# Kernel tuning notes

Hardware: AMD Instinct MI355X
Metric: run time of the kernel (lower is better)

## Reference

```python
import jax, jax.numpy as jnp
import numpy as np

NUM_ITER = 5
DIM = 512
BATCH = 64


def setup_inputs() -> dict:
    key = jax.random.key(0)
    a = jax.random.normal(key, (BATCH, DIM, DIM), dtype=jnp.float32)
    # Symmetric PSD input (covariance-like), as in bilinear pooling; Newton-Schulz
    # requires SPD matrices for convergence.
    x = jnp.einsum('bik,bjk->bij', a, a) / DIM
    I = jnp.eye(DIM, dtype=jnp.float32)
    return {"x": x, "I": I}


def reference(x, I):
    # x: [bs, dim, dim]; I: [dim, dim]
    normA = jnp.sqrt(jnp.sum(x * x, axis=(1, 2), keepdims=True))  # Frobenius norm per matrix
    Y = x / normA
    bs, dim, _ = x.shape
    Z = jnp.broadcast_to(I, (bs, dim, dim))
    Ib = Z
    for _ in range(NUM_ITER):
        T = 0.5 * (3.0 * Ib - jnp.matmul(Z, Y))
        Y = jnp.matmul(Y, T)
        Z = jnp.matmul(T, Z)
    sA = Y * jnp.sqrt(normA)
    return sA
```

## Files before the change

kernel.cpp:

```cpp
#include <hip/hip_runtime.h>
#include <hip/hip_bf16.h>
#include <stdint.h>

#define DIM   512
#define BATCH 64
#define KENC  1024
#define BM    128
#define BN    128
#define BKT   32
#define NKT   16

typedef __attribute__((ext_vector_type(8))) short short8;
typedef __attribute__((ext_vector_type(4))) float floatx4;

__device__ __forceinline__ ushort f2bf(float f) {
    __hip_bfloat16 h = __float2bfloat16(f);
    return *(ushort*)&h;
}
__device__ __forceinline__ float bf2f(ushort u) {
    __hip_bfloat16 h = *(__hip_bfloat16*)&u;
    return (float)h;
}

typedef __attribute__((address_space(3))) uint32_t lds_u32;
typedef const __attribute__((address_space(1))) uint32_t glb_u32;
__device__ __forceinline__ void gload16(const ushort* g, ushort* l) {
    __builtin_amdgcn_global_load_lds((glb_u32*)g, (lds_u32*)l, 16, 0, 0);
}

__global__ __launch_bounds__(256) void norm_partial_kernel(const float* __restrict__ x,
                                                           float* __restrict__ partial) {
    int b = blockIdx.y;
    int i = blockIdx.x;
    const float4* xv = (const float4*)(x + (size_t)b * DIM * DIM + (size_t)i * (DIM * DIM / 16));
    float s = 0.f;
    #pragma unroll
    for (int r = 0; r < 16; ++r) {
        float4 v = xv[r * 256 + threadIdx.x];
        s += v.x * v.x + v.y * v.y + v.z * v.z + v.w * v.w;
    }
    #pragma unroll
    for (int off = 32; off > 0; off >>= 1) s += __shfl_down(s, off, 64);
    __shared__ float red[4];
    int lane = threadIdx.x & 63, wid = threadIdx.x >> 6;
    if (lane == 0) red[wid] = s;
    __syncthreads();
    if (threadIdx.x == 0) partial[b * 16 + i] = red[0] + red[1] + red[2] + red[3];
}

__global__ __launch_bounds__(256) void init_kernel(const float* __restrict__ x,
                                                   const float* __restrict__ partial,
                                                   float* __restrict__ norms,
                                                   ushort* __restrict__ Yenc,
                                                   ushort* __restrict__ Tenc) {
    int b = blockIdx.y;
    float s = 0.f;
    #pragma unroll
    for (int p = 0; p < 16; ++p) s += partial[b * 16 + p];
    float nrm = sqrtf(s);
    if (blockIdx.x == 0 && threadIdx.x == 0) norms[b] = nrm;
    float inv = 1.0f / nrm;
    int idx = (blockIdx.x * 256 + threadIdx.x) * 4;
    int r = idx >> 9;
    int c = idx & 511;
    float4 v = *(const float4*)(x + (size_t)b * DIM * DIM + idx);
    float yv[4] = {v.x * inv, v.y * inv, v.z * inv, v.w * inv};
    size_t base = (size_t)b * DIM * KENC + (size_t)r * KENC;
    ushort yhi[4], ylo[4], thi[4], tlo[4];
    #pragma unroll
    for (int j = 0; j < 4; ++j) {
        float y = yv[j];
        yhi[j] = f2bf(y);
        ylo[j] = f2bf(y - bf2f(yhi[j]));
        float t = ((c + j) == r ? 1.5f : 0.0f) - 0.5f * y;
        thi[j] = f2bf(t);
        tlo[j] = f2bf(t - bf2f(thi[j]));
    }
    *(ushort4*)(Yenc + base + c)       = *(ushort4*)yhi;
    *(ushort4*)(Yenc + base + 512 + c) = *(ushort4*)ylo;
    *(ushort4*)(Tenc + base + c)       = *(ushort4*)thi;
    *(ushort4*)(Tenc + base + 512 + c) = *(ushort4*)tlo;
}

__device__ __forceinline__ void gemm_core(const ushort* Ag, const ushort* Bg,
                                          ushort* sm, floatx4 (&acc)[4][4], int tid) {
    ushort* Ash = sm;
    ushort* Asl = sm + 4096;
    ushort* Bsh = sm + 8192;
    ushort* Bsl = sm + 12288;
    int lane = tid & 63;
    int lane15 = lane & 15, quad = lane >> 4;
    int wave = tid >> 6;
    int wrow = (wave >> 1) * 64, wcol = (wave & 1) * 64;
    int s2 = (lane15 >> 1) & 3;
    int fo = ((quad ^ s2) << 3);

    for (int kt = 0; kt < NKT; ++kt) {
        int k0 = kt * BKT;
        __syncthreads();
        #pragma unroll
        for (int r = 0; r < 2; ++r) {
            int c = r * 256 + tid;
            int row = c >> 2;
            int kc = (((c & 3) ^ ((row >> 1) & 3)) << 3);
            const ushort* ar = Ag + (size_t)row * KENC + k0 + kc;
            const ushort* br = Bg + (size_t)row * KENC + k0 + kc;
            gload16(ar,       &Ash[c * 8]);
            gload16(ar + 512, &Asl[c * 8]);
            gload16(br,       &Bsh[c * 8]);
            gload16(br + 512, &Bsl[c * 8]);
        }
        __syncthreads();
        short8 ah[4], bh[4], xl[4];
        #pragma unroll
        for (int i = 0; i < 4; ++i)
            ah[i] = *(const short8*)&Ash[(wrow + i * 16 + lane15) * BKT + fo];
        #pragma unroll
        for (int j = 0; j < 4; ++j)
            bh[j] = *(const short8*)&Bsh[(wcol + j * 16 + lane15) * BKT + fo];
        #pragma unroll
        for (int i = 0; i < 4; ++i)
            #pragma unroll
            for (int j = 0; j < 4; ++j)
                acc[i][j] = __builtin_amdgcn_mfma_f32_16x16x32_bf16(ah[i], bh[j], acc[i][j], 0, 0, 0);
        #pragma unroll
        for (int j = 0; j < 4; ++j)
            xl[j] = *(const short8*)&Bsl[(wcol + j * 16 + lane15) * BKT + fo];
        #pragma unroll
        for (int i = 0; i < 4; ++i)
            #pragma unroll
            for (int j = 0; j < 4; ++j)
                acc[i][j] = __builtin_amdgcn_mfma_f32_16x16x32_bf16(ah[i], xl[j], acc[i][j], 0, 0, 0);
        #pragma unroll
        for (int i = 0; i < 4; ++i)
            xl[i] = *(const short8*)&Asl[(wrow + i * 16 + lane15) * BKT + fo];
        #pragma unroll
        for (int i = 0; i < 4; ++i)
            #pragma unroll
            for (int j = 0; j < 4; ++j)
                acc[i][j] = __builtin_amdgcn_mfma_f32_16x16x32_bf16(xl[i], bh[j], acc[i][j], 0, 0, 0);
    }
}

__device__ __forceinline__ void store_enc(ushort* Cenc, size_t matoff, int gr, int gc, float v) {
    ushort hi = f2bf(v);
    ushort lo = f2bf(v - bf2f(hi));
    Cenc[matoff + (size_t)gr * KENC + gc] = hi;
    Cenc[matoff + (size_t)gr * KENC + 512 + gc] = lo;
}

template <int MODE>
__global__ __launch_bounds__(256) void gemm_bt(const ushort* __restrict__ A,
                                               const ushort* __restrict__ B,
                                               ushort* __restrict__ Cenc,
                                               float* __restrict__ Cout,
                                               const float* __restrict__ norms) {
    __shared__ __attribute__((aligned(16))) ushort sm[4 * 4096];

    int f = blockIdx.x;
    int xcd = f & 7;
    int g   = f >> 3;
    int b   = xcd + 8 * (g >> 4);
    int t   = g & 15;
    int bm  = t >> 2;
    int bn  = t & 3;

    size_t matoff = (size_t)b * DIM * KENC;
    const ushort* Ag = A + matoff + (size_t)bm * BM * KENC;
    const ushort* Bg = B + matoff + (size_t)bn * BN * KENC;

    int tid = threadIdx.x;
    floatx4 acc[4][4];
    #pragma unroll
    for (int i = 0; i < 4; ++i)
        #pragma unroll
        for (int j = 0; j < 4; ++j)
            acc[i][j] = (floatx4){0.f, 0.f, 0.f, 0.f};

    gemm_core(Ag, Bg, sm, acc, tid);

    int lane = tid & 63;
    int lane15 = lane & 15, quad = lane >> 4;
    int wave = tid >> 6;
    int wrow = (wave >> 1) * 64, wcol = (wave & 1) * 64;
    float scale = (MODE == 2) ? sqrtf(norms[b]) : 0.f;
    #pragma unroll
    for (int i = 0; i < 4; ++i) {
        int gr0 = bm * BM + wrow + i * 16 + quad * 4;
        #pragma unroll
        for (int j = 0; j < 4; ++j) {
            int gc = bn * BN + wcol + j * 16 + lane15;
            #pragma unroll
            for (int rr = 0; rr < 4; ++rr) {
                int gr = gr0 + rr;
                float cv = acc[i][j][rr];
                if (MODE == 0) {
                    store_enc(Cenc, matoff, gr, gc, (gr == gc ? 1.5f : 0.0f) - 0.5f * cv);
                } else if (MODE == 1) {
                    store_enc(Cenc, matoff, gr, gc, cv);
                } else {
                    Cout[(size_t)b * DIM * DIM + (size_t)gr * DIM + gc] = cv * scale;
                }
            }
        }
    }
}

__global__ __launch_bounds__(256) void gemm_yz(const ushort* __restrict__ Y,
                                               const ushort* __restrict__ T,
                                               ushort* __restrict__ Yn,
                                               const ushort* __restrict__ Z,
                                               ushort* __restrict__ Zn) {
    __shared__ __attribute__((aligned(16))) ushort sm[4 * 4096];

    int f0 = blockIdx.x;
    int sel = f0 & 1;
    int f = f0 >> 1;
    int xcd = f & 7;
    int g   = f >> 3;
    int b   = xcd + 8 * (g >> 4);
    int t   = g & 15;
    int bm  = t >> 2;
    int bn  = t & 3;

    size_t matoff = (size_t)b * DIM * KENC;
    const ushort* Abase = sel ? T : Y;
    const ushort* Bbase = sel ? Z : T;
    ushort* Cenc = sel ? Zn : Yn;
    const ushort* Ag = Abase + matoff + (size_t)bm * BM * KENC;
    const ushort* Bg = Bbase + matoff + (size_t)bn * BN * KENC;

    int tid = threadIdx.x;
    floatx4 acc[4][4];
    #pragma unroll
    for (int i = 0; i < 4; ++i)
        #pragma unroll
        for (int j = 0; j < 4; ++j)
            acc[i][j] = (floatx4){0.f, 0.f, 0.f, 0.f};

    gemm_core(Ag, Bg, sm, acc, tid);

    int lane = tid & 63;
    int lane15 = lane & 15, quad = lane >> 4;
    int wave = tid >> 6;
    int wrow = (wave >> 1) * 64, wcol = (wave & 1) * 64;
    #pragma unroll
    for (int i = 0; i < 4; ++i) {
        int gr0 = bm * BM + wrow + i * 16 + quad * 4;
        #pragma unroll
        for (int j = 0; j < 4; ++j) {
            int gc = bn * BN + wcol + j * 16 + lane15;
            #pragma unroll
            for (int rr = 0; rr < 4; ++rr)
                store_enc(Cenc, matoff, gr0 + rr, gc, acc[i][j][rr]);
        }
    }
}

extern "C" void kernel_launch(void* const* d_in, const int* in_sizes, int n_in,
                              void* d_out, int out_size, void* d_ws, size_t ws_size,
                              hipStream_t stream) {
    const float* x = (const float*)d_in[0];
    float* out = (float*)d_out;

    const size_t MATB = (size_t)BATCH * DIM * KENC * sizeof(ushort);
    char* ws = (char*)d_ws;
    ushort* W0 = (ushort*)(ws + 0 * MATB);
    ushort* W1 = (ushort*)(ws + 1 * MATB);
    ushort* W2 = (ushort*)(ws + 2 * MATB);
    float* partial = (float*)(ws + 3 * MATB);
    float* norms   = (float*)(ws + 3 * MATB + 4096);
    ushort* D = (ushort*)d_out;

    dim3 gblk(256);
    dim3 g1(1024);
    dim3 g2(2048);

    norm_partial_kernel<<<dim3(16, BATCH), 256, 0, stream>>>(x, partial);
    init_kernel<<<dim3(256, BATCH), 256, 0, stream>>>(x, partial, norms, W0, W1);

    gemm_bt<1><<<g1, gblk, 0, stream>>>(W0, W1, W2, nullptr, nullptr);
    gemm_bt<0><<<g1, gblk, 0, stream>>>(W1, W2, W0, nullptr, nullptr);
    gemm_bt<1><<<g1, gblk, 0, stream>>>(W2, W0, D, nullptr, nullptr);
    gemm_bt<1><<<g1, gblk, 0, stream>>>(W0, W1, W2, nullptr, nullptr);
    gemm_bt<0><<<g1, gblk, 0, stream>>>(W2, D, W0, nullptr, nullptr);
    gemm_bt<1><<<g1, gblk, 0, stream>>>(D, W0, W1, nullptr, nullptr);
    gemm_bt<1><<<g1, gblk, 0, stream>>>(W0, W2, D, nullptr, nullptr);
    gemm_bt<0><<<g1, gblk, 0, stream>>>(D, W1, W0, nullptr, nullptr);
    gemm_bt<1><<<g1, gblk, 0, stream>>>(W1, W0, W2, nullptr, nullptr);
    gemm_bt<1><<<g1, gblk, 0, stream>>>(W0, D, W1, nullptr, nullptr);
    gemm_bt<0><<<g1, gblk, 0, stream>>>(W1, W2, W0, nullptr, nullptr);
    gemm_bt<2><<<g1, gblk, 0, stream>>>(W2, W0, nullptr, out, norms);
}
```

Baseline: 854.1 us.

## Enlarge GEMM block tile to 256x256 with 16 waves and double-buffered LDS

```diff
diff --git a/kernel.cpp b/kernel.cpp
--- a/kernel.cpp
+++ b/kernel.cpp
@@ -5,10 +5,11 @@
 #define DIM   512
 #define BATCH 64
 #define KENC  1024
-#define BM    128
-#define BN    128
+#define BM    256
+#define BN    256
 #define BKT   32
 #define NKT   16
+#define BUFE  32768
 
 typedef __attribute__((ext_vector_type(8))) short short8;
 typedef __attribute__((ext_vector_type(4))) float floatx4;
@@ -82,64 +83,53 @@
     *(ushort4*)(Tenc + base + 512 + c) = *(ushort4*)tlo;
 }
 
-__device__ __forceinline__ void gemm_core(const ushort* Ag, const ushort* Bg,
-                                          ushort* sm, floatx4 (&acc)[4][4], int tid) {
-    ushort* Ash = sm;
-    ushort* Asl = sm + 4096;
-    ushort* Bsh = sm + 8192;
-    ushort* Bsl = sm + 12288;
-    int lane = tid & 63;
-    int lane15 = lane & 15, quad = lane >> 4;
-    int wave = tid >> 6;
-    int wrow = (wave >> 1) * 64, wcol = (wave & 1) * 64;
-    int s2 = (lane15 >> 1) & 3;
-    int fo = ((quad ^ s2) << 3);
-
-    for (int kt = 0; kt < NKT; ++kt) {
-        int k0 = kt * BKT;
-        __syncthreads();
-        #pragma unroll
-        for (int r = 0; r < 2; ++r) {
-            int c = r * 256 + tid;
-            int row = c >> 2;
-            int kc = (((c & 3) ^ ((row >> 1) & 3)) << 3);
-            const ushort* ar = Ag + (size_t)row * KENC + k0 + kc;
-            const ushort* br = Bg + (size_t)row * KENC + k0 + kc;
-            gload16(ar,       &Ash[c * 8]);
-            gload16(ar + 512, &Asl[c * 8]);
-            gload16(br,       &Bsh[c * 8]);
-            gload16(br + 512, &Bsl[c * 8]);
-        }
-        __syncthreads();
-        short8 ah[4], bh[4], xl[4];
-        #pragma unroll
-        for (int i = 0; i < 4; ++i)
-            ah[i] = *(const short8*)&Ash[(wrow + i * 16 + lane15) * BKT + fo];
-        #pragma unroll
-        for (int j = 0; j < 4; ++j)
-            bh[j] = *(const short8*)&Bsh[(wcol + j * 16 + lane15) * BKT + fo];
-        #pragma unroll
-        for (int i = 0; i < 4; ++i)
-            #pragma unroll
-            for (int j = 0; j < 4; ++j)
-                acc[i][j] = __builtin_amdgcn_mfma_f32_16x16x32_bf16(ah[i], bh[j], acc[i][j], 0, 0, 0);
-        #pragma unroll
-        for (int j = 0; j < 4; ++j)
-            xl[j] = *(const short8*)&Bsl[(wcol + j * 16 + lane15) * BKT + fo];
-        #pragma unroll
-        for (int i = 0; i < 4; ++i)
-            #pragma unroll
-            for (int j = 0; j < 4; ++j)
-                acc[i][j] = __builtin_amdgcn_mfma_f32_16x16x32_bf16(ah[i], xl[j], acc[i][j], 0, 0, 0);
-        #pragma unroll
-        for (int i = 0; i < 4; ++i)
-            xl[i] = *(const short8*)&Asl[(wrow + i * 16 + lane15) * BKT + fo];
-        #pragma unroll
-        for (int i = 0; i < 4; ++i)
-            #pragma unroll
-            for (int j = 0; j < 4; ++j)
-                acc[i][j] = __builtin_amdgcn_mfma_f32_16x16x32_bf16(xl[i], bh[j], acc[i][j], 0, 0, 0);
-    }
+__device__ __forceinline__ void stage_tile(ushort* buf, const ushort* Ag, const ushort* Bg,
+                                           int k0, int tid) {
+    int row = tid >> 2;
+    int pc  = tid & 3;
+    int kc  = ((pc ^ ((row >> 1) & 3)) << 3);
+    const ushort* ar = Ag + (size_t)row * KENC + k0 + kc;
+    const ushort* br = Bg + (size_t)row * KENC + k0 + kc;
+    gload16(ar,       &buf[tid * 8]);
+    gload16(ar + 512, &buf[8192 + tid * 8]);
+    gload16(br,       &buf[16384 + tid * 8]);
+    gload16(br + 512, &buf[24576 + tid * 8]);
+}
+
+__device__ __forceinline__ void compute_tile(const ushort* buf, floatx4 (&acc)[4][4],
+                                             int wrow, int wcol, int lane15, int fo) {
+    const ushort* Ash = buf;
+    const ushort* Asl = buf + 8192;
+    const ushort* Bsh = buf + 16384;
+    const ushort* Bsl = buf + 24576;
+    short8 ah[4], bh[4], xl[4];
+    #pragma unroll
+    for (int i = 0; i < 4; ++i)
+        ah[i] = *(const short8*)&Ash[(wrow + i * 16 + lane15) * BKT + fo];
+    #pragma unroll
+    for (int j = 0; j < 4; ++j)
+        bh[j] = *(const short8*)&Bsh[(wcol + j * 16 + lane15) * BKT + fo];
+    #pragma unroll
+    for (int i = 0; i < 4; ++i)
+        #pragma unroll
+        for (int j = 0; j < 4; ++j)
+            acc[i][j] = __builtin_amdgcn_mfma_f32_16x16x32_bf16(ah[i], bh[j], acc[i][j], 0, 0, 0);
+    #pragma unroll
+    for (int j = 0; j < 4; ++j)
+        xl[j] = *(const short8*)&Bsl[(wcol + j * 16 + lane15) * BKT + fo];
+    #pragma unroll
+    for (int i = 0; i < 4; ++i)
+        #pragma unroll
+        for (int j = 0; j < 4; ++j)
+            acc[i][j] = __builtin_amdgcn_mfma_f32_16x16x32_bf16(ah[i], xl[j], acc[i][j], 0, 0, 0);
+    #pragma unroll
+    for (int i = 0; i < 4; ++i)
+        xl[i] = *(const short8*)&Asl[(wrow + i * 16 + lane15) * BKT + fo];
+    #pragma unroll
+    for (int i = 0; i < 4; ++i)
+        #pragma unroll
+        for (int j = 0; j < 4; ++j)
+            acc[i][j] = __builtin_amdgcn_mfma_f32_16x16x32_bf16(xl[i], bh[j], acc[i][j], 0, 0, 0);
 }
 
 __device__ __forceinline__ void store_enc(ushort* Cenc, size_t matoff, int gr, int gc, float v) {
@@ -150,26 +140,32 @@
 }
 
 template <int MODE>
-__global__ __launch_bounds__(256) void gemm_bt(const ushort* __restrict__ A,
-                                               const ushort* __restrict__ B,
-                                               ushort* __restrict__ Cenc,
-                                               float* __restrict__ Cout,
-                                               const float* __restrict__ norms) {
-    __shared__ __attribute__((aligned(16))) ushort sm[4 * 4096];
+__global__ __launch_bounds__(1024, 4) void gemm_bt(const ushort* __restrict__ A,
+                                                   const ushort* __restrict__ B,
+                                                   ushort* __restrict__ Cenc,
+                                                   float* __restrict__ Cout,
+                                                   const float* __restrict__ norms) {
+    __shared__ __attribute__((aligned(16))) ushort sm[2 * BUFE];
 
     int f = blockIdx.x;
     int xcd = f & 7;
     int g   = f >> 3;
-    int b   = xcd + 8 * (g >> 4);
-    int t   = g & 15;
-    int bm  = t >> 2;
-    int bn  = t & 3;
+    int b   = xcd + 8 * (g >> 2);
+    int t   = g & 3;
+    int bm  = t >> 1;
+    int bn  = t & 1;
 
     size_t matoff = (size_t)b * DIM * KENC;
     const ushort* Ag = A + matoff + (size_t)bm * BM * KENC;
     const ushort* Bg = B + matoff + (size_t)bn * BN * KENC;
 
     int tid = threadIdx.x;
+    int wave = tid >> 6, lane = tid & 63;
+    int lane15 = lane & 15, quad = lane >> 4;
+    int wrow = (wave >> 2) * 64, wcol = (wave & 3) * 64;
+    int s2 = (lane15 >> 1) & 3;
+    int fo = ((quad ^ s2) << 3);
+
     floatx4 acc[4][4];
     #pragma unroll
     for (int i = 0; i < 4; ++i)
@@ -177,12 +173,15 @@
         for (int j = 0; j < 4; ++j)
             acc[i][j] = (floatx4){0.f, 0.f, 0.f, 0.f};
 
-    gemm_core(Ag, Bg, sm, acc, tid);
-
-    int lane = tid & 63;
-    int lane15 = lane & 15, quad = lane >> 4;
-    int wave = tid >> 6;
-    int wrow = (wave >> 1) * 64, wcol = (wave & 1) * 64;
+    stage_tile(sm, Ag, Bg, 0, tid);
+    for (int kt = 0; kt < NKT; ++kt) {
+        ushort* cur = sm + (kt & 1) * BUFE;
+        ushort* nxt = sm + ((kt + 1) & 1) * BUFE;
+        __syncthreads();
+        if (kt + 1 < NKT) stage_tile(nxt, Ag, Bg, (kt + 1) * BKT, tid);
+        compute_tile(cur, acc, wrow, wcol, lane15, fo);
+    }
+
     float scale = (MODE == 2) ? sqrtf(norms[b]) : 0.f;
     #pragma unroll
     for (int i = 0; i < 4; ++i) {
@@ -206,57 +205,6 @@
     }
 }
 
-__global__ __launch_bounds__(256) void gemm_yz(const ushort* __restrict__ Y,
-                                               const ushort* __restrict__ T,
-                                               ushort* __restrict__ Yn,
-                                               const ushort* __restrict__ Z,
-                                               ushort* __restrict__ Zn) {
-    __shared__ __attribute__((aligned(16))) ushort sm[4 * 4096];
-
-    int f0 = blockIdx.x;
-    int sel = f0 & 1;
-    int f = f0 >> 1;
-    int xcd = f & 7;
-    int g   = f >> 3;
-    int b   = xcd + 8 * (g >> 4);
-    int t   = g & 15;
-    int bm  = t >> 2;
-    int bn  = t & 3;
-
-    size_t matoff = (size_t)b * DIM * KENC;
-    const ushort* Abase = sel ? T : Y;
-    const ushort* Bbase = sel ? Z : T;
-    ushort* Cenc = sel ? Zn : Yn;
-    const ushort* Ag = Abase + matoff + (size_t)bm * BM * KENC;
-    const ushort* Bg = Bbase + matoff + (size_t)bn * BN * KENC;
-
-    int tid = threadIdx.x;
-    floatx4 acc[4][4];
-    #pragma unroll
-    for (int i = 0; i < 4; ++i)
-        #pragma unroll
-        for (int j = 0; j < 4; ++j)
-            acc[i][j] = (floatx4){0.f, 0.f, 0.f, 0.f};
-
-    gemm_core(Ag, Bg, sm, acc, tid);
-
-    int lane = tid & 63;
-    int lane15 = lane & 15, quad = lane >> 4;
-    int wave = tid >> 6;
-    int wrow = (wave >> 1) * 64, wcol = (wave & 1) * 64;
-    #pragma unroll
-    for (int i = 0; i < 4; ++i) {
-        int gr0 = bm * BM + wrow + i * 16 + quad * 4;
-        #pragma unroll
-        for (int j = 0; j < 4; ++j) {
-            int gc = bn * BN + wcol + j * 16 + lane15;
-            #pragma unroll
-            for (int rr = 0; rr < 4; ++rr)
-                store_enc(Cenc, matoff, gr0 + rr, gc, acc[i][j][rr]);
-        }
-    }
-}
-
 extern "C" void kernel_launch(void* const* d_in, const int* in_sizes, int n_in,
                               void* d_out, int out_size, void* d_ws, size_t ws_size,
                               hipStream_t stream) {
@@ -272,9 +220,8 @@
     float* norms   = (float*)(ws + 3 * MATB + 4096);
     ushort* D = (ushort*)d_out;
 
-    dim3 gblk(256);
-    dim3 g1(1024);
-    dim3 g2(2048);
+    dim3 gblk(1024);
+    dim3 g1(256);
 
     norm_partial_kernel<<<dim3(16, BATCH), 256, 0, stream>>>(x, partial);
     init_kernel<<<dim3(256, BATCH), 256, 0, stream>>>(x, partial, norms, W0, W1);
```

Measured after the change: 837.2 us. -2.0%, faster.
